# Kernel optimization log

Hardware: AMD Instinct MI355X
Metric: run time of the kernel (lower is better)

## Reference

```python
import jax, jax.numpy as jnp
import numpy as np

DX = 0.1
DY = 0.1
W_B = 1000.0
W_PARALLEL = 1000.0
W_DIV = 100.0
EPS = 1e-10


def setup_inputs() -> dict:
    key = jax.random.key(0)
    k1, k2 = jax.random.split(key)
    outputs = jax.random.normal(k1, (2, 3, 256, 256, 64), dtype=jnp.float32)
    targets = jax.random.normal(k2, (2, 4, 256, 256, 64), dtype=jnp.float32)
    return {"outputs": outputs, "targets": targets}


def _corners(f):
    # 8 shifted views f[..., i:, j:, k:] (with 0 -> [0:-1], 1 -> [1:]) on dims 2,3,4
    s0, s1 = slice(0, -1), slice(1, None)
    return {(i, j, k): f[:, :, (s1 if i else s0), (s1 if j else s0), (s1 if k else s0)]
            for i in (0, 1) for j in (0, 1) for k in (0, 1)}


def _forward(outputs, targets):
    bx_p, by_p, bz_p = outputs[:, 0:1], outputs[:, 1:2], outputs[:, 2:3]
    bx_t, by_t, bz_t = targets[:, 0:1], targets[:, 1:2], targets[:, 2:3]

    loss_b = (jnp.mean((bx_p**2 + by_p**2 - bx_t**2 - by_t**2) ** 2 / (bx_t**2 + by_t**2 + EPS))
              + jnp.mean((bz_p - bz_t) ** 4 / (bz_t**2 + EPS)))
    loss_parallel = jnp.mean((bx_p * by_t - by_p * bx_t) ** 2
                             / (bx_t**2 + by_t**2 + bz_t**2 + EPS))

    bx = _corners(bx_p)
    by = _corners(by_p)
    bz = _corners(bz_p)
    z = _corners(targets[:, 3:4])

    num = (0.25 * (bx[1, 0, 0] + bx[1, 1, 0] + bx[1, 0, 1] + bx[1, 1, 1]) * DY * 0.5 * (z[1, 0, 1] - z[1, 0, 0] + z[1, 1, 1] - z[1, 1, 0])
           - 0.25 * (bx[0, 0, 0] + bx[0, 1, 0] + bx[0, 0, 1] + bx[0, 1, 1]) * DY * 0.5 * (z[0, 0, 1] - z[0, 0, 0] + z[0, 1, 1] - z[0, 1, 0])
           + 0.25 * (by[0, 1, 0] + by[1, 1, 0] + by[0, 1, 1] + by[1, 1, 1]) * DX * 0.5 * (z[0, 1, 1] - z[0, 1, 0] + z[1, 1, 1] - z[1, 1, 0])
           - 0.25 * (by[0, 0, 0] + by[1, 0, 0] + by[0, 0, 1] + by[1, 0, 1]) * DX * 0.5 * (z[0, 0, 1] - z[0, 0, 0] + z[1, 0, 1] - z[1, 0, 0])
           + 0.25 * (bz[0, 0, 1] + bz[0, 1, 1] + bz[1, 0, 1] + bz[1, 1, 1]) * DX * DY
           - 0.25 * (bz[0, 0, 0] + bz[0, 1, 0] + bz[1, 0, 0] + bz[1, 1, 0]) * DX * DY
           + (bx[0, 0, 1] + bx[1, 0, 1] + bx[1, 1, 1]) * DY * (z[0, 0, 1] - z[1, 0, 1]) / 6
           + (bx[0, 1, 1] + bx[1, 1, 1] + bx[1, 0, 1]) * DY * (z[0, 1, 1] - z[1, 1, 1]) / 6
           + (by[1, 0, 1] + by[1, 1, 1] + by[0, 1, 1]) * DX * (z[1, 0, 1] - z[1, 1, 1]) / 6
           + (by[0, 0, 1] + by[0, 1, 1] + by[1, 1, 1]) * DX * (z[0, 0, 1] - z[0, 1, 1]) / 6
           - (bx[0, 0, 0] + bx[1, 0, 0] + bx[1, 1, 0]) * DY * (z[0, 0, 0] - z[1, 0, 0]) / 6
           - (bx[0, 1, 0] + bx[1, 1, 0] + bx[1, 0, 0]) * DY * (z[0, 1, 0] - z[1, 1, 0]) / 6
           - (by[1, 0, 0] + by[1, 1, 0] + by[0, 1, 0]) * DX * (z[1, 0, 0] - z[1, 1, 0]) / 6
           - (by[0, 0, 0] + by[0, 1, 0] + by[1, 1, 0]) * DX * (z[0, 0, 0] - z[0, 1, 0]) / 6)

    bx_c = sum(bx[c] for c in sorted(bx)) * 0.125
    by_c = sum(by[c] for c in sorted(by)) * 0.125
    bz_c = sum(bz[c] for c in sorted(bz)) * 0.125
    den = bx_c**2 + by_c**2 + bz_c**2 + EPS

    loss_div = jnp.mean(num**2 / den) / DX**2 / DY**2

    return (W_B * loss_b + W_PARALLEL * loss_parallel, W_DIV * loss_div)


def reference(outputs, targets):
    return _forward(outputs, targets)
```

## Files before the change

### kernel.cpp

```cpp
#include <hip/hip_runtime.h>

constexpr int B = 2, X = 256, Y = 256, Z = 64;
constexpr int CO = X * Y * Z;
constexpr long long N_PTS   = (long long)B * X * Y * Z;
constexpr long long M_CELLS = (long long)B * (X-1) * (Y-1) * (Z-1);
constexpr int NLINES = B * X * Y;
constexpr int BLOCKS = 2048;
constexpr int TPB = 256;
constexpr int WPB = TPB / 64;
constexpr int TOTAL_WAVES = BLOCKS * WPB;

#define DXc 0.1f
#define DYc 0.1f
#define EPSc 1e-10f

__global__ __launch_bounds__(TPB) void loss_main(const float* __restrict__ outs,
                                                 const float* __restrict__ tgts,
                                                 double* __restrict__ partial) {
    const int lane = threadIdx.x & 63;
    const int wave = threadIdx.x >> 6;
    const int wglobal = blockIdx.x * WPB + wave;

    double s_pt = 0.0;
    double s_dv = 0.0;

    for (int L = wglobal; L < NLINES; L += TOTAL_WAVES) {
        const int b = L >> 16;
        const int r = L & 65535;
        const int x = r >> 8;
        const int y = r & 255;

        const float* ob = outs + ((size_t)b * 3 * CO + (size_t)x * Y * Z + (size_t)y * Z);
        const float* tb = tgts + ((size_t)b * 4 * CO + (size_t)x * Y * Z + (size_t)y * Z);
        const int z = lane;

        const float bxp = ob[0 * CO + z];
        const float byp = ob[1 * CO + z];
        const float bzp = ob[2 * CO + z];
        const float bxt = tb[0 * CO + z];
        const float byt = tb[1 * CO + z];
        const float bzt = tb[2 * CO + z];

        const float bxt2 = bxt * bxt, byt2 = byt * byt, bzt2 = bzt * bzt;
        const float t1 = bxp * bxp + byp * byp - bxt2 - byt2;
        const float e1 = t1 * t1 / (bxt2 + byt2 + EPSc);
        const float dd = bzp - bzt;
        const float dd2 = dd * dd;
        const float e2 = dd2 * dd2 / (bzt2 + EPSc);
        const float cr = bxp * byt - byp * bxt;
        const float e3 = cr * cr / (bxt2 + byt2 + bzt2 + EPSc);
        s_pt += (double)(e1 + e2 + e3);

        if (x < X - 1 && y < Y - 1) {
            const int dxo = Y * Z;
            const int dyo = Z;
            const float bx000 = bxp;
            const float bx100 = ob[0 * CO + dxo + z];
            const float bx010 = ob[0 * CO + dyo + z];
            const float bx110 = ob[0 * CO + dxo + dyo + z];
            const float by000 = byp;
            const float by100 = ob[1 * CO + dxo + z];
            const float by010 = ob[1 * CO + dyo + z];
            const float by110 = ob[1 * CO + dxo + dyo + z];
            const float bz000 = bzp;
            const float bz100 = ob[2 * CO + dxo + z];
            const float bz010 = ob[2 * CO + dyo + z];
            const float bz110 = ob[2 * CO + dxo + dyo + z];
            const float zc000 = tb[3 * CO + z];
            const float zc100 = tb[3 * CO + dxo + z];
            const float zc010 = tb[3 * CO + dyo + z];
            const float zc110 = tb[3 * CO + dxo + dyo + z];

            const float bx001 = __shfl_down(bx000, 1);
            const float bx101 = __shfl_down(bx100, 1);
            const float bx011 = __shfl_down(bx010, 1);
            const float bx111 = __shfl_down(bx110, 1);
            const float by001 = __shfl_down(by000, 1);
            const float by101 = __shfl_down(by100, 1);
            const float by011 = __shfl_down(by010, 1);
            const float by111 = __shfl_down(by110, 1);
            const float bz001 = __shfl_down(bz000, 1);
            const float bz011 = __shfl_down(bz010, 1);
            const float bz101 = __shfl_down(bz100, 1);
            const float bz111 = __shfl_down(bz110, 1);
            const float zc001 = __shfl_down(zc000, 1);
            const float zc101 = __shfl_down(zc100, 1);
            const float zc011 = __shfl_down(zc010, 1);
            const float zc111 = __shfl_down(zc110, 1);

            const float SIXTH = 1.0f / 6.0f;
            float num =
                  0.25f * (bx100 + bx110 + bx101 + bx111) * DYc * 0.5f * (zc101 - zc100 + zc111 - zc110)
                - 0.25f * (bx000 + bx010 + bx001 + bx011) * DYc * 0.5f * (zc001 - zc000 + zc011 - zc010)
                + 0.25f * (by010 + by110 + by011 + by111) * DXc * 0.5f * (zc011 - zc010 + zc111 - zc110)
                - 0.25f * (by000 + by100 + by001 + by101) * DXc * 0.5f * (zc001 - zc000 + zc101 - zc100)
                + 0.25f * (bz001 + bz011 + bz101 + bz111) * DXc * DYc
                - 0.25f * (bz000 + bz010 + bz100 + bz110) * DXc * DYc
                + (bx001 + bx101 + bx111) * DYc * (zc001 - zc101) * SIXTH
                + (bx011 + bx111 + bx101) * DYc * (zc011 - zc111) * SIXTH
                + (by101 + by111 + by011) * DXc * (zc101 - zc111) * SIXTH
                + (by001 + by011 + by111) * DXc * (zc001 - zc011) * SIXTH
                - (bx000 + bx100 + bx110) * DYc * (zc000 - zc100) * SIXTH
                - (bx010 + bx110 + bx100) * DYc * (zc010 - zc110) * SIXTH
                - (by100 + by110 + by010) * DXc * (zc100 - zc110) * SIXTH
                - (by000 + by010 + by110) * DXc * (zc000 - zc010) * SIXTH;

            const float bxc = 0.125f * (bx000 + bx100 + bx010 + bx110 + bx001 + bx101 + bx011 + bx111);
            const float byc = 0.125f * (by000 + by100 + by010 + by110 + by001 + by101 + by011 + by111);
            const float bzc = 0.125f * (bz000 + bz100 + bz010 + bz110 + bz001 + bz101 + bz011 + bz111);
            const float den = bxc * bxc + byc * byc + bzc * bzc + EPSc;

            if (lane < Z - 1) {
                s_dv += (double)(num * num / den);
            }
        }
    }

    for (int off = 32; off > 0; off >>= 1) {
        s_pt += __shfl_down(s_pt, off);
        s_dv += __shfl_down(s_dv, off);
    }

    __shared__ double lds_pt[WPB];
    __shared__ double lds_dv[WPB];
    if (lane == 0) { lds_pt[wave] = s_pt; lds_dv[wave] = s_dv; }
    __syncthreads();
    if (threadIdx.x == 0) {
        double p = 0.0, d = 0.0;
        #pragma unroll
        for (int w = 0; w < WPB; ++w) { p += lds_pt[w]; d += lds_dv[w]; }
        partial[2 * blockIdx.x]     = p;
        partial[2 * blockIdx.x + 1] = d;
    }
}

__global__ __launch_bounds__(256) void loss_finalize(const double* __restrict__ partial,
                                                     float* __restrict__ out) {
    double s0 = 0.0, s1 = 0.0;
    for (int i = threadIdx.x; i < BLOCKS; i += 256) {
        s0 += partial[2 * i];
        s1 += partial[2 * i + 1];
    }
    const int lane = threadIdx.x & 63;
    const int wave = threadIdx.x >> 6;
    for (int off = 32; off > 0; off >>= 1) {
        s0 += __shfl_down(s0, off);
        s1 += __shfl_down(s1, off);
    }
    __shared__ double l0[4], l1[4];
    if (lane == 0) { l0[wave] = s0; l1[wave] = s1; }
    __syncthreads();
    if (threadIdx.x == 0) {
        double p = 0.0, d = 0.0;
        #pragma unroll
        for (int w = 0; w < 4; ++w) { p += l0[w]; d += l1[w]; }
        const double out0 = 1000.0 * (p / (double)N_PTS);
        const double out1 = 100.0 * (d / (double)M_CELLS) / (0.1 * 0.1) / (0.1 * 0.1);
        out[0] = (float)out0;
        out[1] = (float)out1;
    }
}

extern "C" void kernel_launch(void* const* d_in, const int* in_sizes, int n_in,
                              void* d_out, int out_size, void* d_ws, size_t ws_size,
                              hipStream_t stream) {
    const float* outs = (const float*)d_in[0];
    const float* tgts = (const float*)d_in[1];
    float* out = (float*)d_out;
    double* partial = (double*)d_ws;

    loss_main<<<BLOCKS, TPB, 0, stream>>>(outs, tgts, partial);
    loss_finalize<<<1, 256, 0, stream>>>(partial, out);
}
```

Before: 264.2 us.

## March waves along y segments, reusing previous plane loads and shuffles

Each wave now handles a 16-line y segment at fixed x and walks along y, carrying the previous y-plane's values and their z-shifted copies in registers. This removes the redundant reloads of the y+1 neighbours and halves the shuffles per cell, so global loads per point drop from roughly 16 to about 10. The launch now uses one wave per segment instead of a grid-stride loop, giving fewer blocks with longer serial work and a loop-carried register dependency.

```diff
diff --git a/kernel.cpp b/kernel.cpp
--- a/kernel.cpp
+++ b/kernel.cpp
@@ -4,11 +4,13 @@
 constexpr int CO = X * Y * Z;
 constexpr long long N_PTS   = (long long)B * X * Y * Z;
 constexpr long long M_CELLS = (long long)B * (X-1) * (Y-1) * (Z-1);
-constexpr int NLINES = B * X * Y;
-constexpr int BLOCKS = 2048;
+
+constexpr int SEG_LEN    = 16;
+constexpr int SEGS_PER_X = Y / SEG_LEN;
 constexpr int TPB = 256;
 constexpr int WPB = TPB / 64;
-constexpr int TOTAL_WAVES = BLOCKS * WPB;
+constexpr int NSEG   = B * X * SEGS_PER_X;
+constexpr int BLOCKS = NSEG / WPB;
 
 #define DXc 0.1f
 #define DYc 0.1f
@@ -19,100 +21,110 @@
                                                  double* __restrict__ partial) {
     const int lane = threadIdx.x & 63;
     const int wave = threadIdx.x >> 6;
-    const int wglobal = blockIdx.x * WPB + wave;
+    const int seg  = blockIdx.x * WPB + wave;
+
+    const int b  = seg >> 12;
+    const int r  = seg & 4095;
+    const int sy = r >> 8;
+    const int x  = r & 255;
+    const int y0 = sy * SEG_LEN;
+    const bool hasx1 = (x < X - 1);
+    const int nI = (sy == SEGS_PER_X - 1) ? SEG_LEN : SEG_LEN + 1;
+
+    const float* ob = outs + ((size_t)b * 3 * CO + (size_t)x * Y * Z + (size_t)y0 * Z + lane);
+    const float* tb = tgts + ((size_t)b * 4 * CO + (size_t)x * Y * Z + (size_t)y0 * Z + lane);
+    const int DXO = Y * Z;
 
     double s_pt = 0.0;
     double s_dv = 0.0;
 
-    for (int L = wglobal; L < NLINES; L += TOTAL_WAVES) {
-        const int b = L >> 16;
-        const int r = L & 65535;
-        const int x = r >> 8;
-        const int y = r & 255;
+    float p_bx0=0, p_by0=0, p_bz0=0, p_zc0=0;
+    float p_bx1=0, p_by1=0, p_bz1=0, p_zc1=0;
+    float p_bx0s=0, p_by0s=0, p_bz0s=0, p_zc0s=0;
+    float p_bx1s=0, p_by1s=0, p_bz1s=0, p_zc1s=0;
 
-        const float* ob = outs + ((size_t)b * 3 * CO + (size_t)x * Y * Z + (size_t)y * Z);
-        const float* tb = tgts + ((size_t)b * 4 * CO + (size_t)x * Y * Z + (size_t)y * Z);
-        const int z = lane;
+    for (int i = 0; i < nI; ++i) {
+        const int yo = i * Z;
 
-        const float bxp = ob[0 * CO + z];
-        const float byp = ob[1 * CO + z];
-        const float bzp = ob[2 * CO + z];
-        const float bxt = tb[0 * CO + z];
-        const float byt = tb[1 * CO + z];
-        const float bzt = tb[2 * CO + z];
+        const float bx0 = ob[0 * CO + yo];
+        const float by0 = ob[1 * CO + yo];
+        const float bz0 = ob[2 * CO + yo];
+        const float zc0 = tb[3 * CO + yo];
 
-        const float bxt2 = bxt * bxt, byt2 = byt * byt, bzt2 = bzt * bzt;
-        const float t1 = bxp * bxp + byp * byp - bxt2 - byt2;
-        const float e1 = t1 * t1 / (bxt2 + byt2 + EPSc);
-        const float dd = bzp - bzt;
-        const float dd2 = dd * dd;
-        const float e2 = dd2 * dd2 / (bzt2 + EPSc);
-        const float cr = bxp * byt - byp * bxt;
-        const float e3 = cr * cr / (bxt2 + byt2 + bzt2 + EPSc);
-        s_pt += (double)(e1 + e2 + e3);
+        float bx1 = 0, by1 = 0, bz1 = 0, zc1 = 0;
+        if (hasx1) {
+            bx1 = ob[0 * CO + DXO + yo];
+            by1 = ob[1 * CO + DXO + yo];
+            bz1 = ob[2 * CO + DXO + yo];
+            zc1 = tb[3 * CO + DXO + yo];
+        }
 
-        if (x < X - 1 && y < Y - 1) {
-            const int dxo = Y * Z;
-            const int dyo = Z;
-            const float bx000 = bxp;
-            const float bx100 = ob[0 * CO + dxo + z];
-            const float bx010 = ob[0 * CO + dyo + z];
-            const float bx110 = ob[0 * CO + dxo + dyo + z];
-            const float by000 = byp;
-            const float by100 = ob[1 * CO + dxo + z];
-            const float by010 = ob[1 * CO + dyo + z];
-            const float by110 = ob[1 * CO + dxo + dyo + z];
-            const float bz000 = bzp;
-            const float bz100 = ob[2 * CO + dxo + z];
-            const float bz010 = ob[2 * CO + dyo + z];
-            const float bz110 = ob[2 * CO + dxo + dyo + z];
-            const float zc000 = tb[3 * CO + z];
-            const float zc100 = tb[3 * CO + dxo + z];
-            const float zc010 = tb[3 * CO + dyo + z];
-            const float zc110 = tb[3 * CO + dxo + dyo + z];
+        if (i < SEG_LEN) {
+            const float bxt = tb[0 * CO + yo];
+            const float byt = tb[1 * CO + yo];
+            const float bzt = tb[2 * CO + yo];
+            const float bxt2 = bxt * bxt, byt2 = byt * byt, bzt2 = bzt * bzt;
+            const float t1 = bx0 * bx0 + by0 * by0 - bxt2 - byt2;
+            const float e1 = t1 * t1 / (bxt2 + byt2 + EPSc);
+            const float dd = bz0 - bzt;
+            const float dd2 = dd * dd;
+            const float e2 = dd2 * dd2 / (bzt2 + EPSc);
+            const float cr = bx0 * byt - by0 * bxt;
+            const float e3 = cr * cr / (bxt2 + byt2 + bzt2 + EPSc);
+            s_pt += (double)(e1 + e2 + e3);
+        }
 
-            const float bx001 = __shfl_down(bx000, 1);
-            const float bx101 = __shfl_down(bx100, 1);
-            const float bx011 = __shfl_down(bx010, 1);
-            const float bx111 = __shfl_down(bx110, 1);
-            const float by001 = __shfl_down(by000, 1);
-            const float by101 = __shfl_down(by100, 1);
-            const float by011 = __shfl_down(by010, 1);
-            const float by111 = __shfl_down(by110, 1);
-            const float bz001 = __shfl_down(bz000, 1);
-            const float bz011 = __shfl_down(bz010, 1);
-            const float bz101 = __shfl_down(bz100, 1);
-            const float bz111 = __shfl_down(bz110, 1);
-            const float zc001 = __shfl_down(zc000, 1);
-            const float zc101 = __shfl_down(zc100, 1);
-            const float zc011 = __shfl_down(zc010, 1);
-            const float zc111 = __shfl_down(zc110, 1);
+        if (hasx1) {
+            const float bx0s = __shfl_down(bx0, 1);
+            const float by0s = __shfl_down(by0, 1);
+            const float bz0s = __shfl_down(bz0, 1);
+            const float zc0s = __shfl_down(zc0, 1);
+            const float bx1s = __shfl_down(bx1, 1);
+            const float by1s = __shfl_down(by1, 1);
+            const float bz1s = __shfl_down(bz1, 1);
+            const float zc1s = __shfl_down(zc1, 1);
 
-            const float SIXTH = 1.0f / 6.0f;
-            float num =
-                  0.25f * (bx100 + bx110 + bx101 + bx111) * DYc * 0.5f * (zc101 - zc100 + zc111 - zc110)
-                - 0.25f * (bx000 + bx010 + bx001 + bx011) * DYc * 0.5f * (zc001 - zc000 + zc011 - zc010)
-                + 0.25f * (by010 + by110 + by011 + by111) * DXc * 0.5f * (zc011 - zc010 + zc111 - zc110)
-                - 0.25f * (by000 + by100 + by001 + by101) * DXc * 0.5f * (zc001 - zc000 + zc101 - zc100)
-                + 0.25f * (bz001 + bz011 + bz101 + bz111) * DXc * DYc
-                - 0.25f * (bz000 + bz010 + bz100 + bz110) * DXc * DYc
-                + (bx001 + bx101 + bx111) * DYc * (zc001 - zc101) * SIXTH
-                + (bx011 + bx111 + bx101) * DYc * (zc011 - zc111) * SIXTH
-                + (by101 + by111 + by011) * DXc * (zc101 - zc111) * SIXTH
-                + (by001 + by011 + by111) * DXc * (zc001 - zc011) * SIXTH
-                - (bx000 + bx100 + bx110) * DYc * (zc000 - zc100) * SIXTH
-                - (bx010 + bx110 + bx100) * DYc * (zc010 - zc110) * SIXTH
-                - (by100 + by110 + by010) * DXc * (zc100 - zc110) * SIXTH
-                - (by000 + by010 + by110) * DXc * (zc000 - zc010) * SIXTH;
+            if (i >= 1) {
+                const float bx000 = p_bx0,  bx100 = p_bx1,  bx010 = bx0,  bx110 = bx1;
+                const float bx001 = p_bx0s, bx101 = p_bx1s, bx011 = bx0s, bx111 = bx1s;
+                const float by000 = p_by0,  by100 = p_by1,  by010 = by0,  by110 = by1;
+                const float by001 = p_by0s, by101 = p_by1s, by011 = by0s, by111 = by1s;
+                const float bz000 = p_bz0,  bz100 = p_bz1,  bz010 = bz0,  bz110 = bz1;
+                const float bz001 = p_bz0s, bz101 = p_bz1s, bz011 = bz0s, bz111 = bz1s;
+                const float zc000 = p_zc0,  zc100 = p_zc1,  zc010 = zc0,  zc110 = zc1;
+                const float zc001 = p_zc0s, zc101 = p_zc1s, zc011 = zc0s, zc111 = zc1s;
 
-            const float bxc = 0.125f * (bx000 + bx100 + bx010 + bx110 + bx001 + bx101 + bx011 + bx111);
-            const float byc = 0.125f * (by000 + by100 + by010 + by110 + by001 + by101 + by011 + by111);
-            const float bzc = 0.125f * (bz000 + bz100 + bz010 + bz110 + bz001 + bz101 + bz011 + bz111);
-            const float den = bxc * bxc + byc * byc + bzc * bzc + EPSc;
+                const float SIXTH = 1.0f / 6.0f;
+                const float num =
+                      0.25f * (bx100 + bx110 + bx101 + bx111) * DYc * 0.5f * (zc101 - zc100 + zc111 - zc110)
+                    - 0.25f * (bx000 + bx010 + bx001 + bx011) * DYc * 0.5f * (zc001 - zc000 + zc011 - zc010)
+                    + 0.25f * (by010 + by110 + by011 + by111) * DXc * 0.5f * (zc011 - zc010 + zc111 - zc110)
+                    - 0.25f * (by000 + by100 + by001 + by101) * DXc * 0.5f * (zc001 - zc000 + zc101 - zc100)
+                    + 0.25f * (bz001 + bz011 + bz101 + bz111) * DXc * DYc
+                    - 0.25f * (bz000 + bz010 + bz100 + bz110) * DXc * DYc
+                    + (bx001 + bx101 + bx111) * DYc * (zc001 - zc101) * SIXTH
+                    + (bx011 + bx111 + bx101) * DYc * (zc011 - zc111) * SIXTH
+                    + (by101 + by111 + by011) * DXc * (zc101 - zc111) * SIXTH
+                    + (by001 + by011 + by111) * DXc * (zc001 - zc011) * SIXTH
+                    - (bx000 + bx100 + bx110) * DYc * (zc000 - zc100) * SIXTH
+                    - (bx010 + bx110 + bx100) * DYc * (zc010 - zc110) * SIXTH
+                    - (by100 + by110 + by010) * DXc * (zc100 - zc110) * SIXTH
+                    - (by000 + by010 + by110) * DXc * (zc000 - zc010) * SIXTH;
 
-            if (lane < Z - 1) {
-                s_dv += (double)(num * num / den);
+                const float bxc = 0.125f * (bx000 + bx100 + bx010 + bx110 + bx001 + bx101 + bx011 + bx111);
+                const float byc = 0.125f * (by000 + by100 + by010 + by110 + by001 + by101 + by011 + by111);
+                const float bzc = 0.125f * (bz000 + bz100 + bz010 + bz110 + bz001 + bz101 + bz011 + bz111);
+                const float den = bxc * bxc + byc * byc + bzc * bzc + EPSc;
+
+                if (lane < Z - 1) {
+                    s_dv += (double)(num * num / den);
+                }
             }
+
+            p_bx0 = bx0;  p_by0 = by0;  p_bz0 = bz0;  p_zc0 = zc0;
+            p_bx1 = bx1;  p_by1 = by1;  p_bz1 = bz1;  p_zc1 = zc1;
+            p_bx0s = bx0s; p_by0s = by0s; p_bz0s = bz0s; p_zc0s = zc0s;
+            p_bx1s = bx1s; p_by1s = by1s; p_bz1s = bz1s; p_zc1s = zc1s;
         }
     }
 
```

After: 282.3 us. 6.9% more time.

## Vectorize loads with float4 and map each wave to 4 y-rows segment

Applied to the files above, without the earlier changes.

Each wave now handles a segment of four y-rows at one x, with each lane loading float4 chunks along z, replacing the grid-stride loop over single z-lines. Neighbor z values come from within the float4, and only the chunk boundary needs a cross-lane shuffle. The intent is wider, fewer memory instructions, fewer shuffles and less loop overhead. Register pressure rises and the grid grows to one wave per segment, while neighbour loads in x and y are still re-read from global memory rather than shared.

```diff
diff --git a/kernel.cpp b/kernel.cpp
--- a/kernel.cpp
+++ b/kernel.cpp
@@ -2,45 +2,65 @@
 
 constexpr int B = 2, X = 256, Y = 256, Z = 64;
 constexpr int CO = X * Y * Z;
+constexpr int YZ = Y * Z;
 constexpr long long N_PTS   = (long long)B * X * Y * Z;
 constexpr long long M_CELLS = (long long)B * (X-1) * (Y-1) * (Z-1);
-constexpr int NLINES = B * X * Y;
-constexpr int BLOCKS = 2048;
-constexpr int TPB = 256;
-constexpr int WPB = TPB / 64;
-constexpr int TOTAL_WAVES = BLOCKS * WPB;
+
+constexpr int ROWS = 4;
+constexpr int SEGS = Y / ROWS;
+constexpr int TPB  = 256;
+constexpr int WPB  = TPB / 64;
+constexpr int NSEG   = B * SEGS * X;
+constexpr int BLOCKS = NSEG / WPB;
 
 #define DXc 0.1f
 #define DYc 0.1f
 #define EPSc 1e-10f
+
+#define F4C(v, c) (((c) == 0) ? (v).x : ((c) == 1) ? (v).y : ((c) == 2) ? (v).z : (v).w)
 
 __global__ __launch_bounds__(TPB) void loss_main(const float* __restrict__ outs,
                                                  const float* __restrict__ tgts,
                                                  double* __restrict__ partial) {
     const int lane = threadIdx.x & 63;
-    const int wave = threadIdx.x >> 6;
-    const int wglobal = blockIdx.x * WPB + wave;
+    const int wv   = threadIdx.x >> 6;
+    const int seg  = blockIdx.x * WPB + wv;
+
+    const int b  = seg >> 14;
+    const int r  = seg & 16383;
+    const int sy = r >> 8;
+    const int x  = r & 255;
+    const int y0 = sy * ROWS;
+
+    const int row = lane >> 4;
+    const int zi  = (lane & 15) << 2;
+    const int y_own = y0 + row;
+    const int y_up  = (y_own + 1 < Y) ? (y_own + 1) : (Y - 1);
+
+    const float* ob = outs + (size_t)b * 3 * CO;
+    const float* tb = tgts + (size_t)b * 4 * CO;
+    const int off00 = x * YZ + y_own * Z + zi;
+    const int off01 = x * YZ + y_up  * Z + zi;
+    const int off10 = off00 + YZ;
+    const int off11 = off01 + YZ;
+
+    #define LD4(p, off) (*(const float4*)((p) + (off)))
 
     double s_pt = 0.0;
     double s_dv = 0.0;
 
-    for (int L = wglobal; L < NLINES; L += TOTAL_WAVES) {
-        const int b = L >> 16;
-        const int r = L & 65535;
-        const int x = r >> 8;
-        const int y = r & 255;
-
-        const float* ob = outs + ((size_t)b * 3 * CO + (size_t)x * Y * Z + (size_t)y * Z);
-        const float* tb = tgts + ((size_t)b * 4 * CO + (size_t)x * Y * Z + (size_t)y * Z);
-        const int z = lane;
-
-        const float bxp = ob[0 * CO + z];
-        const float byp = ob[1 * CO + z];
-        const float bzp = ob[2 * CO + z];
-        const float bxt = tb[0 * CO + z];
-        const float byt = tb[1 * CO + z];
-        const float bzt = tb[2 * CO + z];
-
+    const float4 obx = LD4(ob, 0 * CO + off00);
+    const float4 oby = LD4(ob, 1 * CO + off00);
+    const float4 obz = LD4(ob, 2 * CO + off00);
+    const float4 tbx = LD4(tb, 0 * CO + off00);
+    const float4 tby = LD4(tb, 1 * CO + off00);
+    const float4 tbz = LD4(tb, 2 * CO + off00);
+    const float4 tzc = LD4(tb, 3 * CO + off00);
+
+    #pragma unroll
+    for (int c = 0; c < 4; ++c) {
+        const float bxp = F4C(obx, c), byp = F4C(oby, c), bzp = F4C(obz, c);
+        const float bxt = F4C(tbx, c), byt = F4C(tby, c), bzt = F4C(tbz, c);
         const float bxt2 = bxt * bxt, byt2 = byt * byt, bzt2 = bzt * bzt;
         const float t1 = bxp * bxp + byp * byp - bxt2 - byt2;
         const float e1 = t1 * t1 / (bxt2 + byt2 + EPSc);
@@ -50,46 +70,71 @@
         const float cr = bxp * byt - byp * bxt;
         const float e3 = cr * cr / (bxt2 + byt2 + bzt2 + EPSc);
         s_pt += (double)(e1 + e2 + e3);
-
-        if (x < X - 1 && y < Y - 1) {
-            const int dxo = Y * Z;
-            const int dyo = Z;
-            const float bx000 = bxp;
-            const float bx100 = ob[0 * CO + dxo + z];
-            const float bx010 = ob[0 * CO + dyo + z];
-            const float bx110 = ob[0 * CO + dxo + dyo + z];
-            const float by000 = byp;
-            const float by100 = ob[1 * CO + dxo + z];
-            const float by010 = ob[1 * CO + dyo + z];
-            const float by110 = ob[1 * CO + dxo + dyo + z];
-            const float bz000 = bzp;
-            const float bz100 = ob[2 * CO + dxo + z];
-            const float bz010 = ob[2 * CO + dyo + z];
-            const float bz110 = ob[2 * CO + dxo + dyo + z];
-            const float zc000 = tb[3 * CO + z];
-            const float zc100 = tb[3 * CO + dxo + z];
-            const float zc010 = tb[3 * CO + dyo + z];
-            const float zc110 = tb[3 * CO + dxo + dyo + z];
-
-            const float bx001 = __shfl_down(bx000, 1);
-            const float bx101 = __shfl_down(bx100, 1);
-            const float bx011 = __shfl_down(bx010, 1);
-            const float bx111 = __shfl_down(bx110, 1);
-            const float by001 = __shfl_down(by000, 1);
-            const float by101 = __shfl_down(by100, 1);
-            const float by011 = __shfl_down(by010, 1);
-            const float by111 = __shfl_down(by110, 1);
-            const float bz001 = __shfl_down(bz000, 1);
-            const float bz011 = __shfl_down(bz010, 1);
-            const float bz101 = __shfl_down(bz100, 1);
-            const float bz111 = __shfl_down(bz110, 1);
-            const float zc001 = __shfl_down(zc000, 1);
-            const float zc101 = __shfl_down(zc100, 1);
-            const float zc011 = __shfl_down(zc010, 1);
-            const float zc111 = __shfl_down(zc110, 1);
-
-            const float SIXTH = 1.0f / 6.0f;
-            float num =
+    }
+
+    if (x < X - 1) {
+        const float4 obx1  = LD4(ob, 0 * CO + off10);
+        const float4 oby1  = LD4(ob, 1 * CO + off10);
+        const float4 obz1  = LD4(ob, 2 * CO + off10);
+        const float4 tzc1  = LD4(tb, 3 * CO + off10);
+        const float4 obxy  = LD4(ob, 0 * CO + off01);
+        const float4 obyy  = LD4(ob, 1 * CO + off01);
+        const float4 obzy  = LD4(ob, 2 * CO + off01);
+        const float4 tzcy  = LD4(tb, 3 * CO + off01);
+        const float4 obxy1 = LD4(ob, 0 * CO + off11);
+        const float4 obyy1 = LD4(ob, 1 * CO + off11);
+        const float4 obzy1 = LD4(ob, 2 * CO + off11);
+        const float4 tzcy1 = LD4(tb, 3 * CO + off11);
+
+        const float n_obx   = __shfl_down(obx.x,   1);
+        const float n_oby   = __shfl_down(oby.x,   1);
+        const float n_obz   = __shfl_down(obz.x,   1);
+        const float n_tzc   = __shfl_down(tzc.x,   1);
+        const float n_obx1  = __shfl_down(obx1.x,  1);
+        const float n_oby1  = __shfl_down(oby1.x,  1);
+        const float n_obz1  = __shfl_down(obz1.x,  1);
+        const float n_tzc1  = __shfl_down(tzc1.x,  1);
+        const float n_obxy  = __shfl_down(obxy.x,  1);
+        const float n_obyy  = __shfl_down(obyy.x,  1);
+        const float n_obzy  = __shfl_down(obzy.x,  1);
+        const float n_tzcy  = __shfl_down(tzcy.x,  1);
+        const float n_obxy1 = __shfl_down(obxy1.x, 1);
+        const float n_obyy1 = __shfl_down(obyy1.x, 1);
+        const float n_obzy1 = __shfl_down(obzy1.x, 1);
+        const float n_tzcy1 = __shfl_down(tzcy1.x, 1);
+
+        const bool yvalid = (y_own < Y - 1);
+        const float SIXTH = 1.0f / 6.0f;
+
+        #pragma unroll
+        for (int c = 0; c < 4; ++c) {
+            const float bx000 = F4C(obx, c),   bx100 = F4C(obx1, c);
+            const float bx010 = F4C(obxy, c),  bx110 = F4C(obxy1, c);
+            const float by000 = F4C(oby, c),   by100 = F4C(oby1, c);
+            const float by010 = F4C(obyy, c),  by110 = F4C(obyy1, c);
+            const float bz000 = F4C(obz, c),   bz100 = F4C(obz1, c);
+            const float bz010 = F4C(obzy, c),  bz110 = F4C(obzy1, c);
+            const float zc000 = F4C(tzc, c),   zc100 = F4C(tzc1, c);
+            const float zc010 = F4C(tzcy, c),  zc110 = F4C(tzcy1, c);
+
+            const float bx001 = (c < 3) ? F4C(obx, c + 1)   : n_obx;
+            const float bx101 = (c < 3) ? F4C(obx1, c + 1)  : n_obx1;
+            const float bx011 = (c < 3) ? F4C(obxy, c + 1)  : n_obxy;
+            const float bx111 = (c < 3) ? F4C(obxy1, c + 1) : n_obxy1;
+            const float by001 = (c < 3) ? F4C(oby, c + 1)   : n_oby;
+            const float by101 = (c < 3) ? F4C(oby1, c + 1)  : n_oby1;
+            const float by011 = (c < 3) ? F4C(obyy, c + 1)  : n_obyy;
+            const float by111 = (c < 3) ? F4C(obyy1, c + 1) : n_obyy1;
+            const float bz001 = (c < 3) ? F4C(obz, c + 1)   : n_obz;
+            const float bz101 = (c < 3) ? F4C(obz1, c + 1)  : n_obz1;
+            const float bz011 = (c < 3) ? F4C(obzy, c + 1)  : n_obzy;
+            const float bz111 = (c < 3) ? F4C(obzy1, c + 1) : n_obzy1;
+            const float zc001 = (c < 3) ? F4C(tzc, c + 1)   : n_tzc;
+            const float zc101 = (c < 3) ? F4C(tzc1, c + 1)  : n_tzc1;
+            const float zc011 = (c < 3) ? F4C(tzcy, c + 1)  : n_tzcy;
+            const float zc111 = (c < 3) ? F4C(tzcy1, c + 1) : n_tzcy1;
+
+            const float num =
                   0.25f * (bx100 + bx110 + bx101 + bx111) * DYc * 0.5f * (zc101 - zc100 + zc111 - zc110)
                 - 0.25f * (bx000 + bx010 + bx001 + bx011) * DYc * 0.5f * (zc001 - zc000 + zc011 - zc010)
                 + 0.25f * (by010 + by110 + by011 + by111) * DXc * 0.5f * (zc011 - zc010 + zc111 - zc110)
@@ -110,7 +155,8 @@
             const float bzc = 0.125f * (bz000 + bz100 + bz010 + bz110 + bz001 + bz101 + bz011 + bz111);
             const float den = bxc * bxc + byc * byc + bzc * bzc + EPSc;
 
-            if (lane < Z - 1) {
+            const bool zvalid = (zi + c) < (Z - 1);
+            if (yvalid && zvalid) {
                 s_dv += (double)(num * num / den);
             }
         }
@@ -123,7 +169,7 @@
 
     __shared__ double lds_pt[WPB];
     __shared__ double lds_dv[WPB];
-    if (lane == 0) { lds_pt[wave] = s_pt; lds_dv[wave] = s_dv; }
+    if (lane == 0) { lds_pt[wv] = s_pt; lds_dv[wv] = s_dv; }
     __syncthreads();
     if (threadIdx.x == 0) {
         double p = 0.0, d = 0.0;
```

New measurement: 265.4 us. About the same (+0.5%).
